# Kernel tuning notes

Measured on AMD Instinct MI355X. Metric: run time of the kernel, lower is better.

The kernel has to match this reference:

```python
import jax, jax.numpy as jnp
import numpy as np

NUM_VERTS = 6890
NUM_FACES = 13776
H, W = 1024, 1024
N, D = 16, 3


def setup_inputs() -> dict:
    key = jax.random.key(0)
    k1, k2, k3, k4, k5 = jax.random.split(key, 5)
    verts_attr = jax.random.normal(k1, (N, NUM_VERTS, D), dtype=jnp.float32)
    face_tensor = jax.random.randint(k2, (NUM_FACES, 3), 0, NUM_VERTS, dtype=jnp.int64)
    pix = jax.random.randint(k3, (H, W), 0, NUM_FACES, dtype=jnp.int64)
    bg = jax.random.uniform(k4, (H, W)) < 0.1
    pix_to_face = jnp.where(bg, jnp.int64(-1), pix)
    # barycentric coords on the simplex
    b = jax.random.uniform(k5, (H, W, 3), dtype=jnp.float32) + 1e-6
    bary_coords = b / jnp.sum(b, axis=-1, keepdims=True)
    return {
        'verts_attr': verts_attr,
        'face_tensor': face_tensor,
        'pix_to_face': pix_to_face,
        'bary_coords': bary_coords,
    }


def reference(verts_attr, face_tensor, pix_to_face, bary_coords):
    n, v, d = verts_attr.shape
    flat = verts_attr.reshape(n * v, d)  # packed (N*V, D)
    # NOTE: original uses (NUM_VERTS - 1) as the per-batch offset (replicated faithfully)
    offsets = (jnp.arange(n, dtype=jnp.int64) * (v - 1))[:, None, None]
    faces_packed = (face_tensor[None] + offsets).reshape(-1, 3)  # (N*F, 3)
    face_attr = flat[faces_packed]  # (N*F, 3, D)
    # NOTE: original repeats pix_to_face across batch without per-batch face offset,
    # so all batches gather from batch-0 face attributes (replicated faithfully).
    mask = pix_to_face >= 0  # (H, W)
    idx = jnp.where(mask, pix_to_face, 0)
    pix_attr = face_attr[idx]  # (H, W, 3, D)
    out_hw = jnp.einsum('hwk,hwkd->hwd', bary_coords, pix_attr)
    out_hw = jnp.where(mask[..., None], out_hw, jnp.zeros((), out_hw.dtype))
    maps_padded = jnp.broadcast_to(out_hw[None], (n,) + out_hw.shape)  # (N, H, W, D)
    return maps_padded
```

## Files before the change

### kernel.cpp

```cpp
#include <hip/hip_runtime.h>
#include <hip/hip_bf16.h>

constexpr int HH    = 1024;
constexpr int WW    = 1024;
constexpr int NPIX  = HH * WW;
constexpr int NB    = 16;
constexpr int PPT   = 4;
constexpr int BLOCK = 256;
constexpr int MAPF4 = NPIX * 3 / 4;
constexpr int REPF4 = (NB - 1) * MAPF4;

typedef float vfloat4 __attribute__((ext_vector_type(4)));

__global__ __launch_bounds__(BLOCK) void uv_compute_map(
    const float* __restrict__ verts,
    const int*   __restrict__ faces,
    const int*   __restrict__ p2f,
    const float* __restrict__ bary,
    float*       __restrict__ out)
{
    const int t  = blockIdx.x * blockDim.x + threadIdx.x;
    const int p0 = t * PPT;
    if (p0 >= NPIX) return;

    const int4 fi = *(const int4*)(p2f + p0);
    const int fidx[PPT] = {fi.x, fi.y, fi.z, fi.w};

    const float4* b4 = (const float4*)(bary + (size_t)p0 * 3);
    const float4 bv0 = b4[0], bv1 = b4[1], bv2 = b4[2];
    const float b[PPT * 3] = {bv0.x, bv0.y, bv0.z, bv0.w,
                              bv1.x, bv1.y, bv1.z, bv1.w,
                              bv2.x, bv2.y, bv2.z, bv2.w};

    alignas(16) float res[PPT * 3];
    #pragma unroll
    for (int i = 0; i < PPT; ++i) {
        const int f = fidx[i];
        float o0 = 0.f, o1 = 0.f, o2 = 0.f;
        if (f >= 0) {
            const int v0 = faces[3 * f + 0];
            const int v1 = faces[3 * f + 1];
            const int v2 = faces[3 * f + 2];
            const float* a0 = verts + 3 * v0;
            const float* a1 = verts + 3 * v1;
            const float* a2 = verts + 3 * v2;
            const float w0 = b[3 * i + 0];
            const float w1 = b[3 * i + 1];
            const float w2 = b[3 * i + 2];
            o0 = w0 * a0[0] + w1 * a1[0] + w2 * a2[0];
            o1 = w0 * a0[1] + w1 * a1[1] + w2 * a2[1];
            o2 = w0 * a0[2] + w1 * a1[2] + w2 * a2[2];
        }
        res[3 * i + 0] = o0;
        res[3 * i + 1] = o1;
        res[3 * i + 2] = o2;
    }

    float4* dst = (float4*)(out + (size_t)p0 * 3);
    const float4* r4 = (const float4*)res;
    dst[0] = r4[0];
    dst[1] = r4[1];
    dst[2] = r4[2];
}

__global__ __launch_bounds__(BLOCK) void uv_replicate(
    const vfloat4* __restrict__ map,
    vfloat4*       __restrict__ dst)
{
    const int tid = blockIdx.x * blockDim.x + threadIdx.x;
    if (tid >= REPF4) return;
    const int m = tid % MAPF4;
    const vfloat4 v = map[m];
    __builtin_nontemporal_store(v, dst + tid);
}

extern "C" void kernel_launch(void* const* d_in, const int* in_sizes, int n_in,
                              void* d_out, int out_size, void* d_ws, size_t ws_size,
                              hipStream_t stream) {
    const float* verts = (const float*)d_in[0];
    const int*   faces = (const int*)d_in[1];
    const int*   p2f   = (const int*)d_in[2];
    const float* bary  = (const float*)d_in[3];
    float*       out   = (float*)d_out;

    const int grid1 = NPIX / PPT / BLOCK;
    uv_compute_map<<<grid1, BLOCK, 0, stream>>>(verts, faces, p2f, bary, out);

    const int grid2 = (REPF4 + BLOCK - 1) / BLOCK;
    uv_replicate<<<grid2, BLOCK, 0, stream>>>((const vfloat4*)out,
                                              (vfloat4*)out + MAPF4);
}
```

Before: 230.2 us.

## Fuse map computation and batch replication into one kernel writing all copies

Each thread now computes its pixels' interpolated attributes and stores them directly into all 16 batch slices with nontemporal stores. This replaces the separate replicate kernel, which reread the computed map and did a modulo per element. A per-block rotation of the batch order spreads concurrent writes across memory regions. In exchange each thread issues many more stores and the grid provides less parallelism per store.

Measured after the change: 317.0 us. +37.7%, slower.

```diff
diff --git a/kernel.cpp b/kernel.cpp
--- a/kernel.cpp
+++ b/kernel.cpp
@@ -7,12 +7,11 @@
 constexpr int NB    = 16;
 constexpr int PPT   = 4;
 constexpr int BLOCK = 256;
-constexpr int MAPF4 = NPIX * 3 / 4;
-constexpr int REPF4 = (NB - 1) * MAPF4;
+constexpr int MAPSZ = NPIX * 3;
 
 typedef float vfloat4 __attribute__((ext_vector_type(4)));
 
-__global__ __launch_bounds__(BLOCK) void uv_compute_map(
+__global__ __launch_bounds__(BLOCK) void uv_fused(
     const float* __restrict__ verts,
     const int*   __restrict__ faces,
     const int*   __restrict__ p2f,
@@ -56,22 +55,19 @@
         res[3 * i + 2] = o2;
     }
 
-    float4* dst = (float4*)(out + (size_t)p0 * 3);
-    const float4* r4 = (const float4*)res;
-    dst[0] = r4[0];
-    dst[1] = r4[1];
-    dst[2] = r4[2];
-}
+    const vfloat4* r4 = (const vfloat4*)res;
+    const vfloat4 r0 = r4[0], r1 = r4[1], r2 = r4[2];
 
-__global__ __launch_bounds__(BLOCK) void uv_replicate(
-    const vfloat4* __restrict__ map,
-    vfloat4*       __restrict__ dst)
-{
-    const int tid = blockIdx.x * blockDim.x + threadIdx.x;
-    if (tid >= REPF4) return;
-    const int m = tid % MAPF4;
-    const vfloat4 v = map[m];
-    __builtin_nontemporal_store(v, dst + tid);
+    const int rot = blockIdx.x & (NB - 1);
+    float* const base = out + (size_t)p0 * 3;
+    #pragma unroll
+    for (int n = 0; n < NB; ++n) {
+        const int bidx = (n + rot) & (NB - 1);
+        vfloat4* dst = (vfloat4*)(base + (size_t)bidx * MAPSZ);
+        __builtin_nontemporal_store(r0, dst + 0);
+        __builtin_nontemporal_store(r1, dst + 1);
+        __builtin_nontemporal_store(r2, dst + 2);
+    }
 }
 
 extern "C" void kernel_launch(void* const* d_in, const int* in_sizes, int n_in,
@@ -83,10 +79,6 @@
     const float* bary  = (const float*)d_in[3];
     float*       out   = (float*)d_out;
 
-    const int grid1 = NPIX / PPT / BLOCK;
-    uv_compute_map<<<grid1, BLOCK, 0, stream>>>(verts, faces, p2f, bary, out);
-
-    const int grid2 = (REPF4 + BLOCK - 1) / BLOCK;
-    uv_replicate<<<grid2, BLOCK, 0, stream>>>((const vfloat4*)out,
-                                              (vfloat4*)out + MAPF4);
+    const int grid = NPIX / PPT / BLOCK;
+    uv_fused<<<grid, BLOCK, 0, stream>>>(verts, faces, p2f, bary, out);
 }
```
